# Kernel tuning notes

Hardware: AMD Instinct MI355X
Metric: run time of the kernel (lower is better)

## Reference

```python
import jax, jax.numpy as jnp
import numpy as np

B = 2048
DIMS = [300, 74, 35]
R = 3
ENC = 150
HID = 32
CAT = ENC * R  # 450


def setup_inputs() -> dict:
    key = jax.random.key(0)
    ks = jax.random.split(key, 32)
    d = {}
    for i, dim in enumerate(DIMS):
        d[f"x{i}"] = jax.random.normal(ks[i], (B, 1, dim), dtype=jnp.float32)
    s = 0.05
    for i, dim in enumerate(DIMS):
        d[f"encW{i}"] = jax.random.normal(ks[3 + 2 * i], (ENC, dim), dtype=jnp.float32) * s
        d[f"encb{i}"] = jax.random.normal(ks[4 + 2 * i], (ENC,), dtype=jnp.float32) * s
    d["affw"] = jax.random.normal(ks[10], (R,), dtype=jnp.float32) * s      # Linear(1,1) weight per branch
    d["Ww"] = jax.random.normal(ks[11], (R, HID, 1), dtype=jnp.float32) * s  # Linear(1,32)
    d["Wc"] = jax.random.normal(ks[12], (R, HID, CAT), dtype=jnp.float32) * s  # Linear(450,32)
    d["Wh"] = jax.random.normal(ks[13], (R, 1, HID), dtype=jnp.float32) * s   # Linear(32,1)
    d["clsW1"] = jax.random.normal(ks[14], (128, CAT), dtype=jnp.float32) * s
    d["clsb1"] = jax.random.normal(ks[15], (128,), dtype=jnp.float32) * s
    d["clsW2"] = jax.random.normal(ks[16], (7, 128), dtype=jnp.float32) * s
    d["clsb2"] = jax.random.normal(ks[17], (7,), dtype=jnp.float32) * s
    return d


def reference(x0, x1, x2, encW0, encb0, encW1, encb1, encW2, encb2,
              affw, Ww, Wc, Wh, clsW1, clsb1, clsW2, clsb2):
    xs = [x0, x1, x2]
    encW = [encW0, encW1, encW2]
    encb = [encb0, encb1, encb2]
    # Encode each modality: [B,1,dim_i] -> [B,1,150]
    enc = [jnp.einsum('btd,ed->bte', xs[i], encW[i]) + encb[i] for i in range(R)]
    feat_n = jnp.concatenate(enc, axis=2)            # [B,1,450]
    scale = 1.0 / jnp.sqrt(jnp.float32(feat_n.shape[1]))  # T=1
    att_feats = []
    for i in range(R):
        enc_t = jnp.swapaxes(enc[i], 1, 2)           # [B,150,1]
        t = jnp.swapaxes(feat_n, 1, 2) * affw[i]     # [B,450,1] (Linear(1,1), no bias)
        # outer product attention: [B,150,1] @ [B,1,450] -> [B,150,450]
        att = jnp.tanh(jnp.matmul(enc_t, jnp.swapaxes(t, 1, 2)) * scale)
        a = jnp.einsum('bec,hc->beh', att, Wc[i])    # [B,150,32]
        b = jnp.matmul(enc_t, Ww[i].T)               # [B,150,1]@[1,32] -> [B,150,32]
        H = jax.nn.relu(a + b)
        out_i = jnp.swapaxes(jnp.matmul(H, Wh[i].T), 1, 2) + enc[i]  # [B,1,150]
        att_feats.append(out_i)
    feats = jnp.concatenate(att_feats, axis=2)       # [B,1,450]
    # classifier (dropout is identity in eval mode)
    h = jnp.einsum('btc,kc->btk', feats, clsW1) + clsb1
    return jnp.einsum('btk,ok->bto', h, clsW2) + clsb2
```

## Files before the change

### kernel.cpp

```cpp
#include <hip/hip_runtime.h>
#include <math.h>

#define NJ 9
#define DEG 17
#define X0f 3.0f

struct Poly { float c[NJ]; };

#define FMA4(A,S,W) do { (A).x = fmaf((S),(W).x,(A).x); (A).y = fmaf((S),(W).y,(A).y); \
                         (A).z = fmaf((S),(W).z,(A).z); (A).w = fmaf((S),(W).w,(A).w); } while(0)

__global__ __launch_bounds__(256) void k_repack(
    const float* __restrict__ Wc, const float* __restrict__ W1,
    const float* __restrict__ eW0, const float* __restrict__ eW1, const float* __restrict__ eW2,
    float* __restrict__ WcT, float* __restrict__ W1T,
    float* __restrict__ Wt0, float* __restrict__ Wt1, float* __restrict__ Wt2) {
    int tid = blockIdx.x * 256 + threadIdx.x;
    int stride = gridDim.x * 256;
    for (int idx = tid; idx < 3 * 464 * 32; idx += stride) {
        int i = idx / (464 * 32); int rem = idx - i * 464 * 32;
        int m = rem >> 5, h = rem & 31;
        float v = 0.f;
        if (m < 456) {
            int seg = m / 152, e = m - seg * 152;
            if (e < 150) v = Wc[((size_t)i * 32 + h) * 450 + seg * 150 + e];
        }
        WcT[idx] = v;
    }
    for (int idx = tid; idx < 456 * 128; idx += stride) {
        int m = idx >> 7, k = idx & 127;
        int seg = m / 152, e = m - seg * 152;
        W1T[idx] = (e < 150) ? W1[k * 450 + seg * 150 + e] : 0.f;
    }
    for (int idx = tid; idx < 304 * 152; idx += stride) {
        int d = idx / 152, e = idx - d * 152;
        Wt0[idx] = (d < 300 && e < 150) ? eW0[e * 300 + d] : 0.f;
    }
    for (int idx = tid; idx < 76 * 152; idx += stride) {
        int d = idx / 152, e = idx - d * 152;
        Wt1[idx] = (d < 74 && e < 150) ? eW1[e * 74 + d] : 0.f;
    }
    for (int idx = tid; idx < 36 * 152; idx += stride) {
        int d = idx / 152, e = idx - d * 152;
        Wt2[idx] = (d < 35 && e < 150) ? eW2[e * 35 + d] : 0.f;
    }
}

__global__ __launch_bounds__(768, 1) void k_fused(
    const float* __restrict__ x0, const float* __restrict__ x1, const float* __restrict__ x2,
    const float* __restrict__ eb0, const float* __restrict__ eb1, const float* __restrict__ eb2,
    const float* __restrict__ Wt0, const float* __restrict__ Wt1, const float* __restrict__ Wt2,
    const float* __restrict__ WcT,
    const float* __restrict__ affw, const float* __restrict__ Ww, const float* __restrict__ Wh,
    const float* __restrict__ W1T, const float* __restrict__ cb1,
    const float* __restrict__ cW2, const float* __restrict__ cb2,
    float* __restrict__ out, Poly pc) {
    __shared__ __align__(16) float xs[8][428];
    __shared__ __align__(16) float feat[8][468];
    __shared__ __align__(16) float fo[8][468];
    __shared__ unsigned smaxu[8];

    int tid = threadIdx.x;
    int b0 = blockIdx.x * 8;

    if (tid < 8) smaxu[tid] = 0u;
    if (tid < 64) feat[tid >> 3][456 + (tid & 7)] = 0.f;
    for (int idx = tid; idx < 8 * 304; idx += 768) {
        int b = idx / 304, d = idx - b * 304;
        xs[b][d] = (d < 300) ? x0[(size_t)(b0 + b) * 300 + d] : 0.f;
    }
    for (int idx = tid; idx < 8 * 76; idx += 768) {
        int b = idx / 76, d = idx - b * 76;
        xs[b][304 + d] = (d < 74) ? x1[(size_t)(b0 + b) * 74 + d] : 0.f;
    }
    for (int idx = tid; idx < 8 * 36; idx += 768) {
        int b = idx / 36, d = idx - b * 36;
        xs[b][380 + d] = (d < 35) ? x2[(size_t)(b0 + b) * 35 + d] : 0.f;
    }
    __syncthreads();

    {
        int tasks[2]; int nt = 1;
        tasks[0] = tid;
        if (tid >= 624) { tasks[nt++] = 768 + (767 - tid); }
        for (int q = 0; q < nt; ++q) {
            int task = tasks[q];
            int b = task & 7, m4 = task >> 3;
            int seg = (m4 >= 76) ? 2 : (m4 >= 38) ? 1 : 0;
            int e4 = m4 - seg * 38;
            const float* eb = seg == 0 ? eb0 : seg == 1 ? eb1 : eb2;
            const float4* Wt4 = (const float4*)(seg == 0 ? Wt0 : seg == 1 ? Wt1 : Wt2) + e4;
            const float4* xr = (const float4*)&xs[b][seg == 0 ? 0 : seg == 1 ? 304 : 380];
            int DP4 = seg == 0 ? 76 : seg == 1 ? 19 : 9;
            int e = e4 * 4;
            float4 acc;
            acc.x = (e     < 150) ? eb[e]     : 0.f;
            acc.y = (e + 1 < 150) ? eb[e + 1] : 0.f;
            acc.z = (e + 2 < 150) ? eb[e + 2] : 0.f;
            acc.w = (e + 3 < 150) ? eb[e + 3] : 0.f;
            for (int d4 = 0; d4 < DP4; ++d4) {
                float4 x4 = xr[d4];
                float4 w0 = Wt4[(d4 * 4 + 0) * 38];
                float4 w1 = Wt4[(d4 * 4 + 1) * 38];
                float4 w2 = Wt4[(d4 * 4 + 2) * 38];
                float4 w3 = Wt4[(d4 * 4 + 3) * 38];
                FMA4(acc, x4.x, w0);
                FMA4(acc, x4.y, w1);
                FMA4(acc, x4.z, w2);
                FMA4(acc, x4.w, w3);
            }
            ((float4*)&feat[b][0])[m4] = acc;
            float mx = fmaxf(fmaxf(fabsf(acc.x), fabsf(acc.y)), fmaxf(fabsf(acc.z), fabsf(acc.w)));
            atomicMax(&smaxu[b], __float_as_uint(mx));
        }
    }
    __syncthreads();

    {
        int w = tid >> 6;
        int i = w >> 2;
        int wp = w & 3;
        int lane = tid & 63;
        int hq = lane & 7, slice = (lane >> 3) & 3, bh = lane >> 5;
        int b = wp * 2 + bh;
        float aff = affw[i];
        const float4* Wb4 = (const float4*)WcT + (size_t)i * 464 * 8 + hq;
        const float4* frow = (const float4*)&feat[b][0];

        float4 acc[NJ];
        #pragma unroll
        for (int J = 0; J < NJ; ++J) acc[J] = make_float4(0.f, 0.f, 0.f, 0.f);

        int m4lo = slice * 29, m4hi = m4lo + 29;
        for (int m4 = m4lo; m4 < m4hi; ++m4) {
            float4 f4 = frow[m4];
            #pragma unroll
            for (int r = 0; r < 4; ++r) {
                float fv = (r == 0) ? f4.x : (r == 1) ? f4.y : (r == 2) ? f4.z : f4.w;
                float g = aff * fv;
                float g2 = g * g;
                float4 wv = Wb4[(m4 * 4 + r) * 8];
                float p = g;
                FMA4(acc[0], p, wv);
                #pragma unroll
                for (int J = 1; J < NJ; ++J) { p *= g2; FMA4(acc[J], p, wv); }
            }
        }
        #pragma unroll
        for (int J = 0; J < NJ; ++J) {
            float cJ = pc.c[J];
            float vx = acc[J].x; vx += __shfl_xor(vx, 8); vx += __shfl_xor(vx, 16);
            float vy = acc[J].y; vy += __shfl_xor(vy, 8); vy += __shfl_xor(vy, 16);
            float vz = acc[J].z; vz += __shfl_xor(vz, 8); vz += __shfl_xor(vz, 16);
            float vw = acc[J].w; vw += __shfl_xor(vw, 8); vw += __shfl_xor(vw, 16);
            acc[J].x = vx * cJ; acc[J].y = vy * cJ; acc[J].z = vz * cJ; acc[J].w = vw * cJ;
        }

        float4 wW4 = ((const float4*)(Ww + i * 32))[hq];
        float4 wH4 = ((const float4*)(Wh + i * 32))[hq];
        float gmax = fabsf(aff) * __uint_as_float(smaxu[b]);
        int e4lo = slice * 10;
        int e4hi = (slice == 3) ? 38 : (e4lo + 10);
        for (int e4 = e4lo; e4 < e4hi; ++e4) {
            float4 s4 = frow[i * 38 + e4];
            float ores[4];
            #pragma unroll
            for (int r = 0; r < 4; ++r) {
                float s = (r == 0) ? s4.x : (r == 1) ? s4.y : (r == 2) ? s4.z : s4.w;
                float4 a4;
                if (fabsf(s) * gmax <= X0f) {
                    float s2 = s * s, p = s;
                    a4.x = acc[0].x * p; a4.y = acc[0].y * p;
                    a4.z = acc[0].z * p; a4.w = acc[0].w * p;
                    #pragma unroll
                    for (int J = 1; J < NJ; ++J) { p *= s2; FMA4(a4, p, acc[J]); }
                } else {
                    a4 = make_float4(0.f, 0.f, 0.f, 0.f);
                    for (int c = 0; c < 456; ++c) {
                        float t = tanhf(s * aff * feat[b][c]);
                        float4 wv = Wb4[c * 8];
                        FMA4(a4, t, wv);
                    }
                }
                float hx = fmaxf(fmaf(s, wW4.x, a4.x), 0.f);
                float hy = fmaxf(fmaf(s, wW4.y, a4.y), 0.f);
                float hz = fmaxf(fmaf(s, wW4.z, a4.z), 0.f);
                float hw = fmaxf(fmaf(s, wW4.w, a4.w), 0.f);
                float csum = hx * wH4.x + hy * wH4.y + hz * wH4.z + hw * wH4.w;
                csum += __shfl_xor(csum, 1);
                csum += __shfl_xor(csum, 2);
                csum += __shfl_xor(csum, 4);
                ores[r] = csum + s;
            }
            if (hq == 0)
                ((float4*)&fo[b][0])[i * 38 + e4] = make_float4(ores[0], ores[1], ores[2], ores[3]);
        }
    }
    __syncthreads();

    {
        int cs = tid >> 8;
        int rr = tid & 255;
        int b = rr >> 5, k4 = rr & 31;
        const float4* W14 = (const float4*)W1T + k4;
        const float4* fr = (const float4*)&fo[b][0];
        float4 a = make_float4(0.f, 0.f, 0.f, 0.f);
        int c4lo = cs * 38, c4hi = c4lo + 38;
        for (int c4 = c4lo; c4 < c4hi; ++c4) {
            float4 fv = fr[c4];
            float4 w0 = W14[(c4 * 4 + 0) * 32];
            float4 w1 = W14[(c4 * 4 + 1) * 32];
            float4 w2 = W14[(c4 * 4 + 2) * 32];
            float4 w3 = W14[(c4 * 4 + 3) * 32];
            FMA4(a, fv.x, w0);
            FMA4(a, fv.y, w1);
            FMA4(a, fv.z, w2);
            FMA4(a, fv.w, w3);
        }
        ((float4*)&xs[0][0])[(cs * 8 + b) * 33 + k4] = a;
    }
    __syncthreads();
    if (tid < 256) {
        int b = tid >> 5, k4 = tid & 31;
        const float4* hp4 = (const float4*)&xs[0][0];
        float4 a = hp4[(b) * 33 + k4];
        float4 p1 = hp4[(8 + b) * 33 + k4];
        float4 p2 = hp4[(16 + b) * 33 + k4];
        float4 bias = ((const float4*)cb1)[k4];
        a.x += p1.x + p2.x + bias.x;
        a.y += p1.y + p2.y + bias.y;
        a.z += p1.z + p2.z + bias.z;
        a.w += p1.w + p2.w + bias.w;
        ((float4*)&feat[b][0])[k4] = a;
    }
    __syncthreads();
    if (tid < 56) {
        int b = tid / 7, o = tid - (tid / 7) * 7;
        const float4* h4 = (const float4*)&feat[b][0];
        const float4* w4 = (const float4*)(cW2 + o * 128);
        float4 a4 = make_float4(0.f, 0.f, 0.f, 0.f);
        #pragma unroll 8
        for (int k4 = 0; k4 < 32; ++k4) {
            float4 h = h4[k4], w = w4[k4];
            a4.x = fmaf(h.x, w.x, a4.x); a4.y = fmaf(h.y, w.y, a4.y);
            a4.z = fmaf(h.z, w.z, a4.z); a4.w = fmaf(h.w, w.w, a4.w);
        }
        out[(size_t)(b0 + b) * 7 + o] = cb2[o] + a4.x + a4.y + a4.z + a4.w;
    }
}

static void make_poly(float* cf) {
    const double a = 3.0;
    const int NQ = 128;
    const double PI = 3.14159265358979323846;
    double b[DEG + 1];
    for (int k = 0; k <= DEG; ++k) b[k] = 0.0;
    for (int m = 0; m < NQ; ++m) {
        double th = PI * (m + 0.5) / NQ;
        double f = tanh(a * cos(th));
        for (int k = 1; k <= DEG; k += 2)
            b[k] += (2.0 / NQ) * f * cos(k * th);
    }
    double Tp[DEG + 1], Tc[DEG + 1], Tn[DEG + 1], mono[DEG + 1];
    for (int j = 0; j <= DEG; ++j) { Tp[j] = 0; Tc[j] = 0; mono[j] = 0; }
    Tp[0] = 1.0;
    Tc[1] = 1.0;
    for (int j = 0; j <= DEG; ++j) mono[j] += b[1] * Tc[j];
    for (int k = 2; k <= DEG; ++k) {
        for (int j = 0; j <= DEG; ++j) Tn[j] = -Tp[j];
        for (int j = 1; j <= DEG; ++j) Tn[j] += 2.0 * Tc[j - 1];
        for (int j = 0; j <= DEG; ++j) { Tp[j] = Tc[j]; Tc[j] = Tn[j]; }
        if (k & 1) for (int j = 0; j <= DEG; ++j) mono[j] += b[k] * Tc[j];
    }
    for (int J = 0; J < NJ; ++J) {
        int j = 2 * J + 1;
        cf[J] = (float)(mono[j] / pow(a, (double)j));
    }
}

extern "C" void kernel_launch(void* const* d_in, const int* in_sizes, int n_in,
                              void* d_out, int out_size, void* d_ws, size_t ws_size,
                              hipStream_t stream) {
    (void)in_sizes; (void)n_in; (void)out_size; (void)ws_size;
    const float* x0    = (const float*)d_in[0];
    const float* x1    = (const float*)d_in[1];
    const float* x2    = (const float*)d_in[2];
    const float* eW0   = (const float*)d_in[3];
    const float* eb0   = (const float*)d_in[4];
    const float* eW1   = (const float*)d_in[5];
    const float* eb1   = (const float*)d_in[6];
    const float* eW2   = (const float*)d_in[7];
    const float* eb2   = (const float*)d_in[8];
    const float* affw  = (const float*)d_in[9];
    const float* Ww    = (const float*)d_in[10];
    const float* Wc    = (const float*)d_in[11];
    const float* Wh    = (const float*)d_in[12];
    const float* cW1   = (const float*)d_in[13];
    const float* cb1   = (const float*)d_in[14];
    const float* cW2   = (const float*)d_in[15];
    const float* cb2   = (const float*)d_in[16];

    float* ws    = (float*)d_ws;
    float* wsWcT = ws;
    float* wsW1T = ws + 44544;
    float* wsWt0 = ws + 102912;
    float* wsWt1 = ws + 149120;
    float* wsWt2 = ws + 160672;

    Poly pc;
    make_poly(pc.c);

    k_repack<<<dim3(96), dim3(256), 0, stream>>>(Wc, cW1, eW0, eW1, eW2,
                                                 wsWcT, wsW1T, wsWt0, wsWt1, wsWt2);
    k_fused<<<dim3(256), dim3(768), 0, stream>>>(x0, x1, x2, eb0, eb1, eb2,
                                                 wsWt0, wsWt1, wsWt2, wsWcT,
                                                 affw, Ww, Wh, wsW1T, cb1, cW2, cb2,
                                                 (float*)d_out, pc);
}
```

Baseline: 77.11 us.

## Halve block batch to 4 rows, lower polynomial degree, compute max in-warp

Rows per block drop from 8 to 4, so there are 512 blocks of 384 threads with launch bounds allowing 3 blocks per CU, which should spread work across more CUs and add occupancy. The odd tanh polynomial goes from degree 17 to 15, removing one accumulator term per element. The shared atomicMax for the per-row feature max is replaced by a max computed during the attention loop and reduced with warp shuffles. Ww/Wh are staged in shared memory and the encoder loop is rewritten per scalar element. The lower degree may reduce accuracy near the fallback threshold.

```diff
diff --git a/kernel.cpp b/kernel.cpp
--- a/kernel.cpp
+++ b/kernel.cpp
@@ -1,9 +1,11 @@
 #include <hip/hip_runtime.h>
 #include <math.h>
 
-#define NJ 9
-#define DEG 17
+#define NJ 8
+#define DEG 15
 #define X0f 3.0f
+#define NB 4
+#define NT 384
 
 struct Poly { float c[NJ]; };
 
@@ -46,7 +48,7 @@
     }
 }
 
-__global__ __launch_bounds__(768, 1) void k_fused(
+__global__ __launch_bounds__(NT, 3) void k_fused(
     const float* __restrict__ x0, const float* __restrict__ x1, const float* __restrict__ x2,
     const float* __restrict__ eb0, const float* __restrict__ eb1, const float* __restrict__ eb2,
     const float* __restrict__ Wt0, const float* __restrict__ Wt1, const float* __restrict__ Wt2,
@@ -55,88 +57,75 @@
     const float* __restrict__ W1T, const float* __restrict__ cb1,
     const float* __restrict__ cW2, const float* __restrict__ cb2,
     float* __restrict__ out, Poly pc) {
-    __shared__ __align__(16) float xs[8][428];
-    __shared__ __align__(16) float feat[8][468];
-    __shared__ __align__(16) float fo[8][468];
-    __shared__ unsigned smaxu[8];
+    __shared__ __align__(16) float xs[NB * 428];
+    __shared__ __align__(16) float featf[NB * 468];
+    __shared__ __align__(16) float fof[NB * 468];
+    __shared__ __align__(16) float wWs[96], wHs[96];
 
     int tid = threadIdx.x;
-    int b0 = blockIdx.x * 8;
-
-    if (tid < 8) smaxu[tid] = 0u;
-    if (tid < 64) feat[tid >> 3][456 + (tid & 7)] = 0.f;
-    for (int idx = tid; idx < 8 * 304; idx += 768) {
-        int b = idx / 304, d = idx - b * 304;
-        xs[b][d] = (d < 300) ? x0[(size_t)(b0 + b) * 300 + d] : 0.f;
-    }
-    for (int idx = tid; idx < 8 * 76; idx += 768) {
-        int b = idx / 76, d = idx - b * 76;
-        xs[b][304 + d] = (d < 74) ? x1[(size_t)(b0 + b) * 74 + d] : 0.f;
-    }
-    for (int idx = tid; idx < 8 * 36; idx += 768) {
-        int b = idx / 36, d = idx - b * 36;
-        xs[b][380 + d] = (d < 35) ? x2[(size_t)(b0 + b) * 35 + d] : 0.f;
-    }
-    __syncthreads();
-
-    {
-        int tasks[2]; int nt = 1;
-        tasks[0] = tid;
-        if (tid >= 624) { tasks[nt++] = 768 + (767 - tid); }
-        for (int q = 0; q < nt; ++q) {
-            int task = tasks[q];
-            int b = task & 7, m4 = task >> 3;
-            int seg = (m4 >= 76) ? 2 : (m4 >= 38) ? 1 : 0;
-            int e4 = m4 - seg * 38;
-            const float* eb = seg == 0 ? eb0 : seg == 1 ? eb1 : eb2;
-            const float4* Wt4 = (const float4*)(seg == 0 ? Wt0 : seg == 1 ? Wt1 : Wt2) + e4;
-            const float4* xr = (const float4*)&xs[b][seg == 0 ? 0 : seg == 1 ? 304 : 380];
-            int DP4 = seg == 0 ? 76 : seg == 1 ? 19 : 9;
-            int e = e4 * 4;
-            float4 acc;
-            acc.x = (e     < 150) ? eb[e]     : 0.f;
-            acc.y = (e + 1 < 150) ? eb[e + 1] : 0.f;
-            acc.z = (e + 2 < 150) ? eb[e + 2] : 0.f;
-            acc.w = (e + 3 < 150) ? eb[e + 3] : 0.f;
-            for (int d4 = 0; d4 < DP4; ++d4) {
-                float4 x4 = xr[d4];
-                float4 w0 = Wt4[(d4 * 4 + 0) * 38];
-                float4 w1 = Wt4[(d4 * 4 + 1) * 38];
-                float4 w2 = Wt4[(d4 * 4 + 2) * 38];
-                float4 w3 = Wt4[(d4 * 4 + 3) * 38];
-                FMA4(acc, x4.x, w0);
-                FMA4(acc, x4.y, w1);
-                FMA4(acc, x4.z, w2);
-                FMA4(acc, x4.w, w3);
-            }
-            ((float4*)&feat[b][0])[m4] = acc;
-            float mx = fmaxf(fmaxf(fabsf(acc.x), fabsf(acc.y)), fmaxf(fabsf(acc.z), fabsf(acc.w)));
-            atomicMax(&smaxu[b], __float_as_uint(mx));
-        }
+    int b0 = blockIdx.x * NB;
+
+    if (tid < 96) { wWs[tid] = Ww[tid]; wHs[tid] = Wh[tid]; }
+    if (tid >= 96 && tid < 144) {
+        int q = tid - 96; int b = q / 12, r = q - b * 12;
+        featf[b * 468 + 456 + r] = 0.f;
+    }
+    for (int idx = tid; idx < NB * 75; idx += NT) {
+        int b = idx / 75, q = idx - b * 75;
+        ((float4*)(xs + b * 428))[q] = ((const float4*)(x0 + (size_t)(b0 + b) * 300))[q];
+    }
+    for (int idx = tid; idx < NB * 74; idx += NT) {
+        int b = idx / 74, d = idx - b * 74;
+        xs[b * 428 + 304 + d] = x1[(size_t)(b0 + b) * 74 + d];
+    }
+    for (int idx = tid; idx < NB * 35; idx += NT) {
+        int b = idx / 35, d = idx - b * 35;
+        xs[b * 428 + 380 + d] = x2[(size_t)(b0 + b) * 35 + d];
+    }
+    __syncthreads();
+
+    for (int task = tid; task < NB * 114; task += NT) {
+        int m4 = task >> 2, b = task & 3;
+        int seg = (m4 >= 76) ? 2 : (m4 >= 38) ? 1 : 0;
+        int e4 = m4 - seg * 38;
+        const float* eb = seg == 0 ? eb0 : seg == 1 ? eb1 : eb2;
+        const float4* W4 = (const float4*)(seg == 0 ? Wt0 : seg == 1 ? Wt1 : Wt2) + e4;
+        const float* xb = xs + b * 428 + (seg == 0 ? 0 : seg == 1 ? 304 : 380);
+        int D = seg == 0 ? 300 : seg == 1 ? 74 : 35;
+        int e = e4 * 4;
+        float4 acc;
+        acc.x = eb[e];
+        acc.y = eb[e + 1];
+        acc.z = (e + 2 < 150) ? eb[e + 2] : 0.f;
+        acc.w = (e + 3 < 150) ? eb[e + 3] : 0.f;
+        #pragma unroll 4
+        for (int d = 0; d < D; ++d) { float xv = xb[d]; float4 wv = W4[d * 38]; FMA4(acc, xv, wv); }
+        ((float4*)(featf + b * 468))[m4] = acc;
     }
     __syncthreads();
 
     {
         int w = tid >> 6;
-        int i = w >> 2;
-        int wp = w & 3;
+        int i = w >> 1, wp = w & 1;
         int lane = tid & 63;
         int hq = lane & 7, slice = (lane >> 3) & 3, bh = lane >> 5;
         int b = wp * 2 + bh;
         float aff = affw[i];
-        const float4* Wb4 = (const float4*)WcT + (size_t)i * 464 * 8 + hq;
-        const float4* frow = (const float4*)&feat[b][0];
+        const float4* Wb4 = (const float4*)WcT + (size_t)i * 3712 + hq;
+        const float4* frow = (const float4*)(featf + b * 468);
 
         float4 acc[NJ];
         #pragma unroll
         for (int J = 0; J < NJ; ++J) acc[J] = make_float4(0.f, 0.f, 0.f, 0.f);
-
-        int m4lo = slice * 29, m4hi = m4lo + 29;
-        for (int m4 = m4lo; m4 < m4hi; ++m4) {
+        float mx = 0.f;
+
+        int m4lo = slice * 29;
+        for (int m4 = m4lo; m4 < m4lo + 29; ++m4) {
             float4 f4 = frow[m4];
             #pragma unroll
             for (int r = 0; r < 4; ++r) {
                 float fv = (r == 0) ? f4.x : (r == 1) ? f4.y : (r == 2) ? f4.z : f4.w;
+                mx = fmaxf(mx, fabsf(fv));
                 float g = aff * fv;
                 float g2 = g * g;
                 float4 wv = Wb4[(m4 * 4 + r) * 8];
@@ -155,10 +144,15 @@
             float vw = acc[J].w; vw += __shfl_xor(vw, 8); vw += __shfl_xor(vw, 16);
             acc[J].x = vx * cJ; acc[J].y = vy * cJ; acc[J].z = vz * cJ; acc[J].w = vw * cJ;
         }
-
-        float4 wW4 = ((const float4*)(Ww + i * 32))[hq];
-        float4 wH4 = ((const float4*)(Wh + i * 32))[hq];
-        float gmax = fabsf(aff) * __uint_as_float(smaxu[b]);
+        mx = fmaxf(mx, __shfl_xor(mx, 1));
+        mx = fmaxf(mx, __shfl_xor(mx, 2));
+        mx = fmaxf(mx, __shfl_xor(mx, 4));
+        mx = fmaxf(mx, __shfl_xor(mx, 8));
+        mx = fmaxf(mx, __shfl_xor(mx, 16));
+        float gmax = fabsf(aff) * mx;
+
+        float4 wW4 = ((const float4*)wWs)[i * 8 + hq];
+        float4 wH4 = ((const float4*)wHs)[i * 8 + hq];
         int e4lo = slice * 10;
         int e4hi = (slice == 3) ? 38 : (e4lo + 10);
         for (int e4 = e4lo; e4 < e4hi; ++e4) {
@@ -177,7 +171,7 @@
                 } else {
                     a4 = make_float4(0.f, 0.f, 0.f, 0.f);
                     for (int c = 0; c < 456; ++c) {
-                        float t = tanhf(s * aff * feat[b][c]);
+                        float t = tanhf(s * aff * featf[b * 468 + c]);
                         float4 wv = Wb4[c * 8];
                         FMA4(a4, t, wv);
                     }
@@ -193,20 +187,20 @@
                 ores[r] = csum + s;
             }
             if (hq == 0)
-                ((float4*)&fo[b][0])[i * 38 + e4] = make_float4(ores[0], ores[1], ores[2], ores[3]);
+                ((float4*)(fof + b * 468))[i * 38 + e4] = make_float4(ores[0], ores[1], ores[2], ores[3]);
         }
     }
     __syncthreads();
 
     {
-        int cs = tid >> 8;
-        int rr = tid & 255;
+        int cs = tid >> 7;
+        int rr = tid & 127;
         int b = rr >> 5, k4 = rr & 31;
         const float4* W14 = (const float4*)W1T + k4;
-        const float4* fr = (const float4*)&fo[b][0];
+        const float4* fr = (const float4*)(fof + b * 468);
         float4 a = make_float4(0.f, 0.f, 0.f, 0.f);
-        int c4lo = cs * 38, c4hi = c4lo + 38;
-        for (int c4 = c4lo; c4 < c4hi; ++c4) {
+        int c4lo = cs * 38;
+        for (int c4 = c4lo; c4 < c4lo + 38; ++c4) {
             float4 fv = fr[c4];
             float4 w0 = W14[(c4 * 4 + 0) * 32];
             float4 w1 = W14[(c4 * 4 + 1) * 32];
@@ -217,35 +211,31 @@
             FMA4(a, fv.z, w2);
             FMA4(a, fv.w, w3);
         }
-        ((float4*)&xs[0][0])[(cs * 8 + b) * 33 + k4] = a;
-    }
-    __syncthreads();
-    if (tid < 256) {
+        ((float4*)xs)[(cs * 4 + b) * 33 + k4] = a;
+    }
+    __syncthreads();
+    if (tid < 128) {
         int b = tid >> 5, k4 = tid & 31;
-        const float4* hp4 = (const float4*)&xs[0][0];
-        float4 a = hp4[(b) * 33 + k4];
-        float4 p1 = hp4[(8 + b) * 33 + k4];
-        float4 p2 = hp4[(16 + b) * 33 + k4];
+        const float4* hp4 = (const float4*)xs;
+        float4 v  = hp4[(0 * 4 + b) * 33 + k4];
+        float4 v1 = hp4[(1 * 4 + b) * 33 + k4];
+        float4 v2 = hp4[(2 * 4 + b) * 33 + k4];
         float4 bias = ((const float4*)cb1)[k4];
-        a.x += p1.x + p2.x + bias.x;
-        a.y += p1.y + p2.y + bias.y;
-        a.z += p1.z + p2.z + bias.z;
-        a.w += p1.w + p2.w + bias.w;
-        ((float4*)&feat[b][0])[k4] = a;
-    }
-    __syncthreads();
-    if (tid < 56) {
+        v.x += v1.x + v2.x + bias.x;
+        v.y += v1.y + v2.y + bias.y;
+        v.z += v1.z + v2.z + bias.z;
+        v.w += v1.w + v2.w + bias.w;
+        ((float4*)(featf + b * 468))[k4] = v;
+    }
+    __syncthreads();
+    if (tid < NB * 7) {
         int b = tid / 7, o = tid - (tid / 7) * 7;
-        const float4* h4 = (const float4*)&feat[b][0];
-        const float4* w4 = (const float4*)(cW2 + o * 128);
-        float4 a4 = make_float4(0.f, 0.f, 0.f, 0.f);
-        #pragma unroll 8
-        for (int k4 = 0; k4 < 32; ++k4) {
-            float4 h = h4[k4], w = w4[k4];
-            a4.x = fmaf(h.x, w.x, a4.x); a4.y = fmaf(h.y, w.y, a4.y);
-            a4.z = fmaf(h.z, w.z, a4.z); a4.w = fmaf(h.w, w.w, a4.w);
-        }
-        out[(size_t)(b0 + b) * 7 + o] = cb2[o] + a4.x + a4.y + a4.z + a4.w;
+        const float* hb = featf + b * 468;
+        const float* w2 = cW2 + o * 128;
+        float acc = cb2[o];
+        #pragma unroll 4
+        for (int k = 0; k < 128; ++k) acc = fmaf(hb[k], w2[k], acc);
+        out[(size_t)(b0 + b) * 7 + o] = acc;
     }
 }
 
@@ -312,8 +302,8 @@
 
     k_repack<<<dim3(96), dim3(256), 0, stream>>>(Wc, cW1, eW0, eW1, eW2,
                                                  wsWcT, wsW1T, wsWt0, wsWt1, wsWt2);
-    k_fused<<<dim3(256), dim3(768), 0, stream>>>(x0, x1, x2, eb0, eb1, eb2,
-                                                 wsWt0, wsWt1, wsWt2, wsWcT,
-                                                 affw, Ww, Wh, wsW1T, cb1, cW2, cb2,
-                                                 (float*)d_out, pc);
+    k_fused<<<dim3(512), dim3(NT), 0, stream>>>(x0, x1, x2, eb0, eb1, eb2,
+                                                wsWt0, wsWt1, wsWt2, wsWcT,
+                                                affw, Ww, Wh, wsW1T, cb1, cW2, cb2,
+                                                (float*)d_out, pc);
 }
```

Result: slower. 111.1 us, median of 2 (+44.1%).
